# Kernel tuning notes

Measured on AMD Instinct MI355X. Metric: run time of the kernel, lower is better.

## Reference

```python
import jax, jax.numpy as jnp
import numpy as np


def dht(x):
    # Discrete Hartley transform along last axis: DHT(x) = Re(FFT) - Im(FFT)
    X = jnp.fft.fft(x, axis=-1)
    return (X.real - X.imag).astype(x.dtype)


def idht(x):
    # Inverse DHT = DHT / N
    n = x.shape[-1]
    return dht(x) / n


def setup_inputs() -> dict:
    key = jax.random.key(0)
    k1, k2 = jax.random.split(key)
    B, Cin, Cout, N, M = 16, 64, 64, 16384, 64
    x = jax.random.normal(k1, (B, Cin, N), dtype=jnp.float32)
    scale = 1.0 / (Cin * Cout)
    weights1 = scale * jax.random.uniform(k2, (Cout, Cin, M), dtype=jnp.float32)
    return {"x": x, "weights1": weights1, "modes1": M}


def reference(x, weights1, modes1):
    # x: [B, Cin, N]; weights1: [Cout, Cin, M]
    B, Cin, N = x.shape
    Cout = weights1.shape[0]
    x_ht = dht(x)                                  # [B, Cin, N]
    # Mode-wise channel contraction on the first `modes1` Hartley modes
    low = jnp.einsum('bim,oim->bom', x_ht[:, :, :modes1], weights1)  # [B, Cout, M]
    out_ht = jnp.zeros((B, Cout, N), dtype=x.dtype).at[:, :, :modes1].set(low)
    return idht(out_ht)                            # [B, Cout, N]
```

## Files before the change

### kernel.cpp

```cpp
#include <hip/hip_runtime.h>
#include <math.h>

#define N_FFT 16384
#define HALF 8192
#define ROWS 1024
#define KS_A 64
#define KR_A 128
#define CHUNK 32
#define NMASK 16383


__global__ __launch_bounds__(256) void k_tab(float* __restrict__ castab,
                                             float* __restrict__ costab) {
    int i = blockIdx.x * 256 + threadIdx.x;
    double ang = 6.283185307179586476925287 * (double)i / (double)N_FFT;
    double c = cos(ang), s = sin(ang);
    castab[i] = (float)(c + s);
    costab[i] = (float)(2.0 * c);
}

__global__ __launch_bounds__(512, 4) void kA(const float* __restrict__ x,
                                             const float* __restrict__ castab,
                                             const float* __restrict__ costab,
                                             float* __restrict__ partial) {
    const int rb = blockIdx.x & 7;
    const int ks = blockIdx.x >> 3;
    const int rowbase = rb << 7;
    const int kbase = ks * KR_A;

    __shared__ float xs[CHUNK][2][128];

    const int t   = threadIdx.x;
    const int wq  = __builtin_amdgcn_readfirstlane(t >> 6);
    const int lam = t & 63;
    const int c0  = wq * 8;
    const int p   = wq >> 2;
    const int r2  = lam * 2;
    const int mbase = (wq < 4) ? (wq << 4) : (((wq - 4) << 4) + 1);

    float k2[8], cA[8], cB[8];
#pragma unroll
    for (int j = 0; j < 8; ++j) {
        const int m = mbase + 2 * j;
        k2[j] = costab[m];
        cB[j] = castab[((kbase - 1) * m) & NMASK];
        cA[j] = castab[(kbase * m) & NMASK];
    }

    float acc0[8], acc1[8];
#pragma unroll
    for (int j = 0; j < 8; ++j) { acc0[j] = 0.f; acc1[j] = 0.f; }

    for (int ch = 0; ch < KR_A / CHUNK; ++ch) {
        const int k0 = kbase + ch * CHUNK;
        if (ch) __syncthreads();
#pragma unroll
        for (int it = 0; it < 2; ++it) {
            const int idx = it * 512 + t;
            const int r = idx >> 3, kq = idx & 7;
            const float4 a4 = *reinterpret_cast<const float4*>(
                &x[(size_t)(rowbase + r) * N_FFT + k0 + kq * 4]);
            const float4 b4 = *reinterpret_cast<const float4*>(
                &x[(size_t)(rowbase + r) * N_FFT + k0 + kq * 4 + HALF]);
            const int rsw = r ^ (kq << 1);
#pragma unroll
            for (int u = 0; u < 4; ++u) {
                const float a = reinterpret_cast<const float*>(&a4)[u];
                const float b = reinterpret_cast<const float*>(&b4)[u];
                xs[kq * 4 + u][0][rsw] = a + b;
                xs[kq * 4 + u][1][rsw] = a - b;
            }
        }
        __syncthreads();

        for (int k = 0; k < CHUNK; k += 2) {
            {
                const int rd = r2 ^ ((k >> 2) << 1);
                const float2 s2 = *reinterpret_cast<const float2*>(&xs[k][p][rd]);
#pragma unroll
                for (int j = 0; j < 8; ++j) {
                    acc0[j] = fmaf(s2.x, cA[j], acc0[j]);
                    acc1[j] = fmaf(s2.y, cA[j], acc1[j]);
                    cB[j] = fmaf(k2[j], cA[j], -cB[j]);
                }
            }
            {
                const int rd = r2 ^ (((k + 1) >> 2) << 1);
                const float2 s2 = *reinterpret_cast<const float2*>(&xs[k + 1][p][rd]);
#pragma unroll
                for (int j = 0; j < 8; ++j) {
                    acc0[j] = fmaf(s2.x, cB[j], acc0[j]);
                    acc1[j] = fmaf(s2.y, cB[j], acc1[j]);
                    cA[j] = fmaf(k2[j], cB[j], -cA[j]);
                }
            }
        }
    }

#pragma unroll
    for (int i = 0; i < 2; ++i) {
        float* pp = &partial[((size_t)ks << 16) +
                             (size_t)(rowbase + r2 + i) * 64 + c0];
        const float* a = i ? acc1 : acc0;
        *reinterpret_cast<float4*>(pp) =
            make_float4(a[0], a[1], a[2], a[3]);
        *reinterpret_cast<float4*>(pp + 4) =
            make_float4(a[4], a[5], a[6], a[7]);
    }
}

__global__ __launch_bounds__(256) void kR(const float* __restrict__ partial,
                                          float* __restrict__ xh) {
    const int idx = blockIdx.x * 256 + threadIdx.x;
    const int r = idx >> 6, c = idx & 63;
    const int m = (c < 32) ? (2 * c) : (2 * (c - 32) + 1);
    float a0 = 0.f, a1 = 0.f, a2 = 0.f, a3 = 0.f;
#pragma unroll 4
    for (int sp = 0; sp < KS_A; sp += 4) {
        a0 += partial[((size_t)(sp + 0) << 16) + idx];
        a1 += partial[((size_t)(sp + 1) << 16) + idx];
        a2 += partial[((size_t)(sp + 2) << 16) + idx];
        a3 += partial[((size_t)(sp + 3) << 16) + idx];
    }
    xh[(r << 6) + m] = (a0 + a1) + (a2 + a3);
}

__global__ __launch_bounds__(256) void kB(const float* __restrict__ xh,
                                          const float* __restrict__ w,
                                          float* __restrict__ lowT) {
    const int b  = blockIdx.x >> 4;
    const int og = blockIdx.x & 15;
    const int o  = og * 4 + (threadIdx.x >> 6);
    const int m  = threadIdx.x & 63;
    float a0 = 0.f, a1 = 0.f, a2 = 0.f, a3 = 0.f;
#pragma unroll 4
    for (int i = 0; i < 64; i += 4) {
        a0 = fmaf(xh[(size_t)((b * 64 + i + 0) << 6) + m], w[(size_t)((o * 64 + i + 0) << 6) + m], a0);
        a1 = fmaf(xh[(size_t)((b * 64 + i + 1) << 6) + m], w[(size_t)((o * 64 + i + 1) << 6) + m], a1);
        a2 = fmaf(xh[(size_t)((b * 64 + i + 2) << 6) + m], w[(size_t)((o * 64 + i + 2) << 6) + m], a2);
        a3 = fmaf(xh[(size_t)((b * 64 + i + 3) << 6) + m], w[(size_t)((o * 64 + i + 3) << 6) + m], a3);
    }
    lowT[(size_t)m * ROWS + b * 64 + o] = ((a0 + a1) + (a2 + a3)) * (1.0f / (float)N_FFT);
}

__global__ __launch_bounds__(256, 4) void kC(const float* __restrict__ lowT,
                                             const float* __restrict__ castab,
                                             const float* __restrict__ costab,
                                             float* __restrict__ out) {
    const int nb = blockIdx.x & 127;
    const int rb = blockIdx.x >> 7;
    const int t  = threadIdx.x;
    const int wq = __builtin_amdgcn_readfirstlane(t >> 6);
    const int r0 = rb * 64 + wq * 16;
    const int n  = (nb << 6) + (t & 63);

    const float k2 = costab[n];
    float ce = 1.0f;
    float co = castab[n];

    float se[16], so[16];
#pragma unroll
    for (int j = 0; j < 16; ++j) { se[j] = 0.f; so[j] = 0.f; }

#pragma unroll 2
    for (int g = 0; g < 32; ++g) {
        const float* le = lowT + ((size_t)(2 * g) << 10) + r0;
        const float* lo = le + ROWS;
#pragma unroll
        for (int j = 0; j < 16; ++j) {
            se[j] = fmaf(ce, le[j], se[j]);
            so[j] = fmaf(co, lo[j], so[j]);
        }
        ce = fmaf(k2, co, -ce);
        co = fmaf(k2, ce, -co);
    }

#pragma unroll
    for (int j = 0; j < 16; ++j) {
        const size_t row = (size_t)r0 + j;
        out[row * N_FFT + n]        = se[j] + so[j];
        out[row * N_FFT + HALF + n] = se[j] - so[j];
    }
}

extern "C" void kernel_launch(void* const* d_in, const int* in_sizes, int n_in,
                              void* d_out, int out_size, void* d_ws, size_t ws_size,
                              hipStream_t stream) {
    const float* x = (const float*)d_in[0];
    const float* w = (const float*)d_in[1];
    float* out = (float*)d_out;
    float* ws  = (float*)d_ws;

    float* castab  = ws;
    float* costab  = ws + 16384;
    float* partial = ws + 32768;
    float* xh      = ws + 4227072;
    float* lowT    = ws + 4292608;

    k_tab<<<64, 256, 0, stream>>>(castab, costab);
    kA<<<512, 512, 0, stream>>>(x, castab, costab, partial);
    kR<<<256, 256, 0, stream>>>(partial, xh);
    kB<<<256, 256, 0, stream>>>(xh, w, lowT);
    kC<<<2048, 256, 0, stream>>>(lowT, castab, costab, out);
}
```

Measured before the change: 66.86 us.

## Double-buffer input staging in kA and restructure kC with LDS-staged lowT and float4 stores

kA now double-buffers its shared-memory tile. The next chunk's global loads are issued into registers before the current chunk's FMA loop and written to the alternate buffer afterwards, so load latency overlaps compute and one barrier per chunk is removed. kC is reorganised so each block handles 16 rows by 256 columns. It stages the needed lowT slice in LDS, and each thread computes 4 rows by 4 consecutive outputs, writing them with float4 stores. This trades more registers and LDS use for better load latency hiding and wider, coalesced output writes.

```diff
diff --git a/kernel.cpp b/kernel.cpp
--- a/kernel.cpp
+++ b/kernel.cpp
@@ -28,7 +28,7 @@
     const int rowbase = rb << 7;
     const int kbase = ks * KR_A;
 
-    __shared__ float xs[CHUNK][2][128];
+    __shared__ float xs[2][CHUNK][2][128];
 
     const int t   = threadIdx.x;
     const int wq  = __builtin_amdgcn_readfirstlane(t >> 6);
@@ -51,32 +51,45 @@
 #pragma unroll
     for (int j = 0; j < 8; ++j) { acc0[j] = 0.f; acc1[j] = 0.f; }
 
+    float4 xa[2], xb[2];
+
+#define LOADREG(K0)                                                           \
+    _Pragma("unroll")                                                         \
+    for (int it = 0; it < 2; ++it) {                                          \
+        const int idx = it * 512 + t;                                         \
+        const int r = idx >> 3, kq = idx & 7;                                 \
+        const float* src = &x[(size_t)(rowbase + r) * N_FFT + (K0) + kq * 4]; \
+        xa[it] = *reinterpret_cast<const float4*>(src);                       \
+        xb[it] = *reinterpret_cast<const float4*>(src + HALF);                \
+    }
+
+#define WRITEBUF(B)                                                           \
+    _Pragma("unroll")                                                         \
+    for (int it = 0; it < 2; ++it) {                                          \
+        const int idx = it * 512 + t;                                         \
+        const int r = idx >> 3, kq = idx & 7;                                 \
+        const int rsw = r ^ (kq << 1);                                        \
+        _Pragma("unroll")                                                     \
+        for (int u = 0; u < 4; ++u) {                                         \
+            const float a = reinterpret_cast<const float*>(&xa[it])[u];       \
+            const float b = reinterpret_cast<const float*>(&xb[it])[u];       \
+            xs[B][kq * 4 + u][0][rsw] = a + b;                                \
+            xs[B][kq * 4 + u][1][rsw] = a - b;                                \
+        }                                                                     \
+    }
+
+    LOADREG(kbase);
+    WRITEBUF(0);
+    __syncthreads();
+
     for (int ch = 0; ch < KR_A / CHUNK; ++ch) {
-        const int k0 = kbase + ch * CHUNK;
-        if (ch) __syncthreads();
-#pragma unroll
-        for (int it = 0; it < 2; ++it) {
-            const int idx = it * 512 + t;
-            const int r = idx >> 3, kq = idx & 7;
-            const float4 a4 = *reinterpret_cast<const float4*>(
-                &x[(size_t)(rowbase + r) * N_FFT + k0 + kq * 4]);
-            const float4 b4 = *reinterpret_cast<const float4*>(
-                &x[(size_t)(rowbase + r) * N_FFT + k0 + kq * 4 + HALF]);
-            const int rsw = r ^ (kq << 1);
-#pragma unroll
-            for (int u = 0; u < 4; ++u) {
-                const float a = reinterpret_cast<const float*>(&a4)[u];
-                const float b = reinterpret_cast<const float*>(&b4)[u];
-                xs[kq * 4 + u][0][rsw] = a + b;
-                xs[kq * 4 + u][1][rsw] = a - b;
-            }
-        }
-        __syncthreads();
+        const int buf = ch & 1;
+        if (ch + 1 < KR_A / CHUNK) { LOADREG(kbase + (ch + 1) * CHUNK); }
 
         for (int k = 0; k < CHUNK; k += 2) {
             {
                 const int rd = r2 ^ ((k >> 2) << 1);
-                const float2 s2 = *reinterpret_cast<const float2*>(&xs[k][p][rd]);
+                const float2 s2 = *reinterpret_cast<const float2*>(&xs[buf][k][p][rd]);
 #pragma unroll
                 for (int j = 0; j < 8; ++j) {
                     acc0[j] = fmaf(s2.x, cA[j], acc0[j]);
@@ -86,7 +99,7 @@
             }
             {
                 const int rd = r2 ^ (((k + 1) >> 2) << 1);
-                const float2 s2 = *reinterpret_cast<const float2*>(&xs[k + 1][p][rd]);
+                const float2 s2 = *reinterpret_cast<const float2*>(&xs[buf][k + 1][p][rd]);
 #pragma unroll
                 for (int j = 0; j < 8; ++j) {
                     acc0[j] = fmaf(s2.x, cB[j], acc0[j]);
@@ -95,7 +108,14 @@
                 }
             }
         }
-    }
+
+        if (ch + 1 < KR_A / CHUNK) {
+            WRITEBUF(buf ^ 1);
+            __syncthreads();
+        }
+    }
+#undef LOADREG
+#undef WRITEBUF
 
 #pragma unroll
     for (int i = 0; i < 2; ++i) {
@@ -147,39 +167,69 @@
                                              const float* __restrict__ castab,
                                              const float* __restrict__ costab,
                                              float* __restrict__ out) {
-    const int nb = blockIdx.x & 127;
-    const int rb = blockIdx.x >> 7;
+    const int rb = blockIdx.x >> 5;
+    const int nb = blockIdx.x & 31;
+    const int rowbase = rb << 4;
+    const int n0 = nb << 8;
+
+    __shared__ float ls[64][16];
+
     const int t  = threadIdx.x;
-    const int wq = __builtin_amdgcn_readfirstlane(t >> 6);
-    const int r0 = rb * 64 + wq * 16;
-    const int n  = (nb << 6) + (t & 63);
-
-    const float k2 = costab[n];
-    float ce = 1.0f;
-    float co = castab[n];
-
-    float se[16], so[16];
-#pragma unroll
-    for (int j = 0; j < 16; ++j) { se[j] = 0.f; so[j] = 0.f; }
-
-#pragma unroll 2
+    const int rg = __builtin_amdgcn_readfirstlane(t >> 6);
+    const int nl = t & 63;
+    const int n  = n0 + nl * 4;
+
+#pragma unroll
+    for (int it = 0; it < 4; ++it) {
+        const int f = it * 256 + t;
+        const int m = f >> 4, r = f & 15;
+        ls[m][r] = lowT[((size_t)m << 10) + rowbase + r];
+    }
+    __syncthreads();
+
+    float k2[4], ce[4], co[4];
+#pragma unroll
+    for (int j = 0; j < 4; ++j) {
+        k2[j] = costab[n + j];
+        ce[j] = 1.0f;
+        co[j] = castab[n + j];
+    }
+
+    float se[4][4], so[4][4];
+#pragma unroll
+    for (int r = 0; r < 4; ++r)
+#pragma unroll
+        for (int j = 0; j < 4; ++j) { se[r][j] = 0.f; so[r][j] = 0.f; }
+
+#pragma unroll 4
     for (int g = 0; g < 32; ++g) {
-        const float* le = lowT + ((size_t)(2 * g) << 10) + r0;
-        const float* lo = le + ROWS;
-#pragma unroll
-        for (int j = 0; j < 16; ++j) {
-            se[j] = fmaf(ce, le[j], se[j]);
-            so[j] = fmaf(co, lo[j], so[j]);
+        const float4 le = *reinterpret_cast<const float4*>(&ls[2 * g][rg * 4]);
+        const float4 lo = *reinterpret_cast<const float4*>(&ls[2 * g + 1][rg * 4]);
+        const float lev[4] = {le.x, le.y, le.z, le.w};
+        const float lov[4] = {lo.x, lo.y, lo.z, lo.w};
+#pragma unroll
+        for (int r = 0; r < 4; ++r)
+#pragma unroll
+            for (int j = 0; j < 4; ++j) {
+                se[r][j] = fmaf(ce[j], lev[r], se[r][j]);
+                so[r][j] = fmaf(co[j], lov[r], so[r][j]);
+            }
+#pragma unroll
+        for (int j = 0; j < 4; ++j) {
+            ce[j] = fmaf(k2[j], co[j], -ce[j]);
+            co[j] = fmaf(k2[j], ce[j], -co[j]);
         }
-        ce = fmaf(k2, co, -ce);
-        co = fmaf(k2, ce, -co);
-    }
-
-#pragma unroll
-    for (int j = 0; j < 16; ++j) {
-        const size_t row = (size_t)r0 + j;
-        out[row * N_FFT + n]        = se[j] + so[j];
-        out[row * N_FFT + HALF + n] = se[j] - so[j];
+    }
+
+#pragma unroll
+    for (int r = 0; r < 4; ++r) {
+        const size_t row = (size_t)rowbase + rg * 4 + r;
+        *reinterpret_cast<float4*>(&out[row * N_FFT + n]) =
+            make_float4(se[r][0] + so[r][0], se[r][1] + so[r][1],
+                        se[r][2] + so[r][2], se[r][3] + so[r][3]);
+        *reinterpret_cast<float4*>(&out[row * N_FFT + HALF + n]) =
+            make_float4(se[r][0] - so[r][0], se[r][1] - so[r][1],
+                        se[r][2] - so[r][2], se[r][3] - so[r][3]);
     }
 }
 
```

After: 81.57 us. 22.0% more time.
